# Kernel optimization log

Hardware: AMD Instinct MI355X
Metric: run time of the kernel (lower is better)

Reference implementation:

```python
import jax, jax.numpy as jnp
import numpy as np

S, N, E = 128, 512, 256   # msa depth, residues, msa embedding
P, C = 32, 128            # product embedding, pair embedding
EPS = 1e-5


def setup_inputs() -> dict:
    key = jax.random.key(0)
    ks = jax.random.split(key, 7)
    sc_e = 1.0 / np.sqrt(E)
    sc_p = 1.0 / np.sqrt(P)
    return {
        "msa_rep": jax.random.normal(ks[0], (S, N, E), dtype=jnp.float32),
        "ln_gamma": jnp.ones((E,), dtype=jnp.float32),
        "ln_beta": jnp.zeros((E,), dtype=jnp.float32),
        "Wa": jax.random.uniform(ks[1], (E, P), minval=-sc_e, maxval=sc_e, dtype=jnp.float32),
        "ba": jax.random.uniform(ks[2], (P,), minval=-sc_e, maxval=sc_e, dtype=jnp.float32),
        "Wb": jax.random.uniform(ks[3], (E, P), minval=-sc_e, maxval=sc_e, dtype=jnp.float32),
        "bb": jax.random.uniform(ks[4], (P,), minval=-sc_e, maxval=sc_e, dtype=jnp.float32),
        "Wp": jax.random.uniform(ks[5], (P, C), minval=-sc_p, maxval=sc_p, dtype=jnp.float32),
        "bp": jax.random.uniform(ks[6], (C,), minval=-sc_p, maxval=sc_p, dtype=jnp.float32),
    }


def reference(msa_rep, ln_gamma, ln_beta, Wa, ba, Wb, bb, Wp, bp):
    # LayerNorm over msa embedding dim
    mu = jnp.mean(msa_rep, axis=-1, keepdims=True)
    var = jnp.var(msa_rep, axis=-1, keepdims=True)
    x = (msa_rep - mu) / jnp.sqrt(var + EPS) * ln_gamma + ln_beta
    # dual projections: [S, N, P]
    a = x @ Wa + ba
    b = x @ Wb + bb
    # outer-product mean over MSA depth S without materializing [S, P, N, N]:
    # outer[n, m, p] = mean_s a[s, n, p] * b[s, m, p]  -> batched GEMM over p
    outer = jnp.einsum('snp,smp->nmp', a, b) / a.shape[0]
    # project product channels to pair embedding: [N, N, C]
    return outer @ Wp + bp
```

## Files before the change

kernel.cpp:

```cpp
#include <hip/hip_runtime.h>

#define S_DEPTH 128
#define N_RES   512
#define E_DIM   256
#define P_DIM   32
#define C_DIM   128

typedef short bh8 __attribute__((ext_vector_type(8)));
typedef float fx4 __attribute__((ext_vector_type(4)));

__device__ __forceinline__ unsigned short f2bf(float x){
    unsigned int u = __builtin_bit_cast(unsigned int, x);
    u += 0x7fffu + ((u >> 16) & 1u);
    return (unsigned short)(u >> 16);
}

__global__ void prep_kernel(const float* __restrict__ Wa, const float* __restrict__ Wb,
                            const float* __restrict__ Wp,
                            unsigned short* __restrict__ WaT, unsigned short* __restrict__ WbT,
                            unsigned short* __restrict__ WpT){
    int t = threadIdx.x;
    for (int i = 0; i < 32; ++i){
        int idx = i * 256 + t;
        int p = idx >> 8, e = idx & 255;
        WaT[idx] = f2bf(Wa[e * P_DIM + p]);
        WbT[idx] = f2bf(Wb[e * P_DIM + p]);
    }
    for (int i = 0; i < 16; ++i){
        int idx = i * 256 + t;
        int c = idx >> 5, p = idx & 31;
        WpT[idx] = f2bf(Wp[p * C_DIM + c]);
    }
}

__global__ __launch_bounds__(256) void lnproj_kernel(
    const float* __restrict__ x, const float* __restrict__ gamma, const float* __restrict__ beta,
    const unsigned short* __restrict__ WaT, const unsigned short* __restrict__ WbT,
    const float* __restrict__ ba, const float* __restrict__ bb,
    unsigned short* __restrict__ aT, unsigned short* __restrict__ bT)
{
    __shared__ __align__(16) char smem[S_DEPTH * E_DIM * 2];
    const int n0   = blockIdx.x;
    const int tid  = threadIdx.x;
    const int lane = tid & 63;
    const int w    = tid >> 6;
    const int l15  = lane & 15;
    const int lq   = lane >> 4;

    const float4 g4 = *(const float4*)(gamma + lane * 4);
    const float4 b4 = *(const float4*)(beta  + lane * 4);

    for (int rr = 0; rr < 32; ++rr){
        int s = w * 32 + rr;
        float4 v = *(const float4*)(x + ((size_t)(s * N_RES + n0)) * E_DIM + lane * 4);
        float sum = v.x + v.y + v.z + v.w;
        float sq  = v.x*v.x + v.y*v.y + v.z*v.z + v.w*v.w;
        #pragma unroll
        for (int m = 1; m < 64; m <<= 1){
            sum += __shfl_xor(sum, m);
            sq  += __shfl_xor(sq,  m);
        }
        float mu  = sum * (1.0f / E_DIM);
        float inv = rsqrtf(sq * (1.0f / E_DIM) - mu * mu + 1e-5f);
        ushort4 pk;
        pk.x = f2bf((v.x - mu) * inv * g4.x + b4.x);
        pk.y = f2bf((v.y - mu) * inv * g4.y + b4.y);
        pk.z = f2bf((v.z - mu) * inv * g4.z + b4.z);
        pk.w = f2bf((v.w - mu) * inv * g4.w + b4.w);
        int boff = s * 512 + lane * 8;
        boff ^= (s & 7) << 4;
        *(ushort4*)(smem + boff) = pk;
    }
    __syncthreads();

    fx4 accA[2][2], accB[2][2];
    #pragma unroll
    for (int st = 0; st < 2; ++st)
        #pragma unroll
        for (int pt = 0; pt < 2; ++pt){
            accA[st][pt] = fx4{0.f, 0.f, 0.f, 0.f};
            accB[st][pt] = fx4{0.f, 0.f, 0.f, 0.f};
        }

    #pragma unroll
    for (int ks = 0; ks < 8; ++ks){
        bh8 wa[2], wb[2];
        #pragma unroll
        for (int pt = 0; pt < 2; ++pt){
            int off = (pt * 16 + l15) * E_DIM + ks * 32 + lq * 8;
            wa[pt] = *(const bh8*)(WaT + off);
            wb[pt] = *(const bh8*)(WbT + off);
        }
        #pragma unroll
        for (int st = 0; st < 2; ++st){
            int srow = (w * 2 + st) * 16 + l15;
            int boff = srow * 512 + (ks * 32 + lq * 8) * 2;
            boff ^= (srow & 7) << 4;
            bh8 xf = *(const bh8*)(smem + boff);
            #pragma unroll
            for (int pt = 0; pt < 2; ++pt){
                accA[st][pt] = __builtin_amdgcn_mfma_f32_16x16x32_bf16(wa[pt], xf, accA[st][pt], 0, 0, 0);
                accB[st][pt] = __builtin_amdgcn_mfma_f32_16x16x32_bf16(wb[pt], xf, accB[st][pt], 0, 0, 0);
            }
        }
    }

    #pragma unroll
    for (int st = 0; st < 2; ++st){
        int s = (w * 2 + st) * 16 + l15;
        #pragma unroll
        for (int pt = 0; pt < 2; ++pt){
            #pragma unroll
            for (int j = 0; j < 4; ++j){
                int p = pt * 16 + lq * 4 + j;
                size_t o = ((size_t)p * N_RES + n0) * S_DEPTH + s;
                aT[o] = f2bf(accA[st][pt][j] + ba[p]);
                bT[o] = f2bf(accB[st][pt][j] + bb[p]);
            }
        }
    }
}

__global__ __launch_bounds__(512) void outer_kernel(
    const unsigned short* __restrict__ aT, const unsigned short* __restrict__ bT,
    const unsigned short* __restrict__ WpT, const float* __restrict__ bp,
    float* __restrict__ out)
{
    __shared__ __align__(16) char smem[1024 * 64];
    const int tn = blockIdx.x >> 4, tm = blockIdx.x & 15;
    const int n0 = tn * 32, m0 = tm * 32;
    const int tid  = threadIdx.x;
    const int lane = tid & 63;
    const int w    = tid >> 6;
    const int l15  = lane & 15;
    const int lq   = lane >> 4;

    #pragma unroll
    for (int q = 0; q < 4; ++q){
        int p = w * 4 + q;
        fx4 acc[2][2];
        #pragma unroll
        for (int ti = 0; ti < 2; ++ti)
            #pragma unroll
            for (int tj = 0; tj < 2; ++tj)
                acc[ti][tj] = fx4{0.f, 0.f, 0.f, 0.f};

        #pragma unroll
        for (int ks = 0; ks < 4; ++ks){
            bh8 af[2], bfv[2];
            #pragma unroll
            for (int t = 0; t < 2; ++t){
                af[t]  = *(const bh8*)(aT + ((size_t)p * N_RES + n0 + t * 16 + l15) * S_DEPTH + ks * 32 + lq * 8);
                bfv[t] = *(const bh8*)(bT + ((size_t)p * N_RES + m0 + t * 16 + l15) * S_DEPTH + ks * 32 + lq * 8);
            }
            #pragma unroll
            for (int ti = 0; ti < 2; ++ti)
                #pragma unroll
                for (int tj = 0; tj < 2; ++tj)
                    acc[ti][tj] = __builtin_amdgcn_mfma_f32_16x16x32_bf16(af[ti], bfv[tj], acc[ti][tj], 0, 0, 0);
        }
        #pragma unroll
        for (int ti = 0; ti < 2; ++ti)
            #pragma unroll
            for (int tj = 0; tj < 2; ++tj)
                #pragma unroll
                for (int j = 0; j < 4; ++j){
                    int nloc = ti * 16 + lq * 4 + j;
                    int mloc = tj * 16 + l15;
                    int nm = nloc * 32 + mloc;
                    *(unsigned short*)(smem + nm * 64 + p * 2) =
                        f2bf(acc[ti][tj][j] * (1.0f / S_DEPTH));
                }
    }
    __syncthreads();

    bh8   wpf[8];
    float bpv[8];
    #pragma unroll
    for (int ct = 0; ct < 8; ++ct){
        wpf[ct] = *(const bh8*)(WpT + (ct * 16 + l15) * P_DIM + lq * 8);
        bpv[ct] = bp[ct * 16 + l15];
    }
    #pragma unroll
    for (int mi = 0; mi < 8; ++mi){
        int mt = w * 8 + mi;
        bh8 of = *(const bh8*)(smem + (mt * 16 + l15) * 64 + lq * 16);
        #pragma unroll
        for (int ct = 0; ct < 8; ++ct){
            fx4 d = __builtin_amdgcn_mfma_f32_16x16x32_bf16(
                        of, wpf[ct], fx4{0.f, 0.f, 0.f, 0.f}, 0, 0, 0);
            #pragma unroll
            for (int j = 0; j < 4; ++j){
                int nm = mt * 16 + lq * 4 + j;
                int n = n0 + (nm >> 5), m = m0 + (nm & 31);
                out[((size_t)n * N_RES + m) * C_DIM + ct * 16 + l15] = d[j] + bpv[ct];
            }
        }
    }
}

extern "C" void kernel_launch(void* const* d_in, const int* in_sizes, int n_in,
                              void* d_out, int out_size, void* d_ws, size_t ws_size,
                              hipStream_t stream){
    const float* msa   = (const float*)d_in[0];
    const float* gamma = (const float*)d_in[1];
    const float* beta  = (const float*)d_in[2];
    const float* Wa    = (const float*)d_in[3];
    const float* ba    = (const float*)d_in[4];
    const float* Wb    = (const float*)d_in[5];
    const float* bb    = (const float*)d_in[6];
    const float* Wp    = (const float*)d_in[7];
    const float* bp    = (const float*)d_in[8];
    float* out = (float*)d_out;

    unsigned short* ws  = (unsigned short*)d_ws;
    unsigned short* aT  = ws;
    unsigned short* bT  = ws + 2097152;
    unsigned short* WaT = ws + 4194304;
    unsigned short* WbT = WaT + 8192;
    unsigned short* WpT = WbT + 8192;

    prep_kernel<<<1, 256, 0, stream>>>(Wa, Wb, Wp, WaT, WbT, WpT);
    lnproj_kernel<<<N_RES, 256, 0, stream>>>(msa, gamma, beta, WaT, WbT, ba, bb, aT, bT);
    outer_kernel<<<256, 512, 0, stream>>>(aT, bT, WpT, bp, out);
}
```

Before: 79.43 us.

## Retile all three kernels: parallel prep, split-S lnproj, 32x16 outer tiles

The prep kernel now runs on 48 blocks with one element per thread instead of a single serial block. The LN+projection kernel splits S across two blocks per residue and swaps the MFMA operand order so the output comes out as vectorized ushort4 stores. The outer kernel uses 32x16 tiles with 256 threads and grid swizzling, with each wave owning 8 product channels so the bf16 intermediate can be packed and written in 16-byte chunks into padded LDS. Output uses nontemporal stores with simpler addressing. These changes aim to raise occupancy, improve store coalescing and cut LDS write traffic, at the cost of more re-reading of the a/b operands per output tile.

Measured after the change: 102.5 us. 1.29x slower.

```diff
diff --git a/kernel.cpp b/kernel.cpp
--- a/kernel.cpp
+++ b/kernel.cpp
@@ -19,28 +19,27 @@
                             const float* __restrict__ Wp,
                             unsigned short* __restrict__ WaT, unsigned short* __restrict__ WbT,
                             unsigned short* __restrict__ WpT){
-    int t = threadIdx.x;
-    for (int i = 0; i < 32; ++i){
-        int idx = i * 256 + t;
-        int p = idx >> 8, e = idx & 255;
-        WaT[idx] = f2bf(Wa[e * P_DIM + p]);
-        WbT[idx] = f2bf(Wb[e * P_DIM + p]);
-    }
-    for (int i = 0; i < 16; ++i){
-        int idx = i * 256 + t;
-        int c = idx >> 5, p = idx & 31;
-        WpT[idx] = f2bf(Wp[p * C_DIM + c]);
-    }
-}
-
-__global__ __launch_bounds__(256) void lnproj_kernel(
+    int tid = blockIdx.x * 256 + threadIdx.x;
+    if (tid < 8192){
+        int p = tid >> 8, e = tid & 255;
+        WaT[tid] = f2bf(Wa[e * P_DIM + p]);
+        WbT[tid] = f2bf(Wb[e * P_DIM + p]);
+    } else {
+        int i = tid - 8192;
+        int c = i >> 5, p = i & 31;
+        WpT[i] = f2bf(Wp[p * C_DIM + c]);
+    }
+}
+
+__global__ __launch_bounds__(256, 4) void lnproj_kernel(
     const float* __restrict__ x, const float* __restrict__ gamma, const float* __restrict__ beta,
     const unsigned short* __restrict__ WaT, const unsigned short* __restrict__ WbT,
     const float* __restrict__ ba, const float* __restrict__ bb,
     unsigned short* __restrict__ aT, unsigned short* __restrict__ bT)
 {
-    __shared__ __align__(16) char smem[S_DEPTH * E_DIM * 2];
+    __shared__ __align__(16) char smem[64 * 512];
     const int n0   = blockIdx.x;
+    const int sh   = blockIdx.y;
     const int tid  = threadIdx.x;
     const int lane = tid & 63;
     const int w    = tid >> 6;
@@ -50,8 +49,9 @@
     const float4 g4 = *(const float4*)(gamma + lane * 4);
     const float4 b4 = *(const float4*)(beta  + lane * 4);
 
-    for (int rr = 0; rr < 32; ++rr){
-        int s = w * 32 + rr;
+    for (int rr = 0; rr < 16; ++rr){
+        int s_loc = w * 16 + rr;
+        int s     = sh * 64 + s_loc;
         float4 v = *(const float4*)(x + ((size_t)(s * N_RES + n0)) * E_DIM + lane * 4);
         float sum = v.x + v.y + v.z + v.w;
         float sq  = v.x*v.x + v.y*v.y + v.z*v.z + v.w*v.w;
@@ -67,111 +67,99 @@
         pk.y = f2bf((v.y - mu) * inv * g4.y + b4.y);
         pk.z = f2bf((v.z - mu) * inv * g4.z + b4.z);
         pk.w = f2bf((v.w - mu) * inv * g4.w + b4.w);
-        int boff = s * 512 + lane * 8;
-        boff ^= (s & 7) << 4;
+        int boff = s_loc * 512 + lane * 8;
+        boff ^= (s_loc & 7) << 4;
         *(ushort4*)(smem + boff) = pk;
     }
     __syncthreads();
 
-    fx4 accA[2][2], accB[2][2];
-    #pragma unroll
-    for (int st = 0; st < 2; ++st)
-        #pragma unroll
-        for (int pt = 0; pt < 2; ++pt){
-            accA[st][pt] = fx4{0.f, 0.f, 0.f, 0.f};
-            accB[st][pt] = fx4{0.f, 0.f, 0.f, 0.f};
-        }
+    fx4 accA[2], accB[2];
+    #pragma unroll
+    for (int pt = 0; pt < 2; ++pt){
+        accA[pt] = fx4{0.f, 0.f, 0.f, 0.f};
+        accB[pt] = fx4{0.f, 0.f, 0.f, 0.f};
+    }
+    const int srow = w * 16 + l15;
 
     #pragma unroll
     for (int ks = 0; ks < 8; ++ks){
-        bh8 wa[2], wb[2];
+        int boff = srow * 512 + (ks * 32 + lq * 8) * 2;
+        boff ^= (srow & 7) << 4;
+        bh8 xf = *(const bh8*)(smem + boff);
         #pragma unroll
         for (int pt = 0; pt < 2; ++pt){
             int off = (pt * 16 + l15) * E_DIM + ks * 32 + lq * 8;
-            wa[pt] = *(const bh8*)(WaT + off);
-            wb[pt] = *(const bh8*)(WbT + off);
-        }
-        #pragma unroll
-        for (int st = 0; st < 2; ++st){
-            int srow = (w * 2 + st) * 16 + l15;
-            int boff = srow * 512 + (ks * 32 + lq * 8) * 2;
-            boff ^= (srow & 7) << 4;
-            bh8 xf = *(const bh8*)(smem + boff);
-            #pragma unroll
-            for (int pt = 0; pt < 2; ++pt){
-                accA[st][pt] = __builtin_amdgcn_mfma_f32_16x16x32_bf16(wa[pt], xf, accA[st][pt], 0, 0, 0);
-                accB[st][pt] = __builtin_amdgcn_mfma_f32_16x16x32_bf16(wb[pt], xf, accB[st][pt], 0, 0, 0);
-            }
-        }
-    }
-
-    #pragma unroll
-    for (int st = 0; st < 2; ++st){
-        int s = (w * 2 + st) * 16 + l15;
-        #pragma unroll
-        for (int pt = 0; pt < 2; ++pt){
-            #pragma unroll
-            for (int j = 0; j < 4; ++j){
-                int p = pt * 16 + lq * 4 + j;
-                size_t o = ((size_t)p * N_RES + n0) * S_DEPTH + s;
-                aT[o] = f2bf(accA[st][pt][j] + ba[p]);
-                bT[o] = f2bf(accB[st][pt][j] + bb[p]);
-            }
-        }
-    }
-}
-
-__global__ __launch_bounds__(512) void outer_kernel(
+            bh8 wa = *(const bh8*)(WaT + off);
+            bh8 wb = *(const bh8*)(WbT + off);
+            accA[pt] = __builtin_amdgcn_mfma_f32_16x16x32_bf16(xf, wa, accA[pt], 0, 0, 0);
+            accB[pt] = __builtin_amdgcn_mfma_f32_16x16x32_bf16(xf, wb, accB[pt], 0, 0, 0);
+        }
+    }
+
+    #pragma unroll
+    for (int pt = 0; pt < 2; ++pt){
+        int p = pt * 16 + l15;
+        float bav = ba[p], bbv = bb[p];
+        int s_base = sh * 64 + w * 16 + lq * 4;
+        size_t o = ((size_t)p * N_RES + n0) * S_DEPTH + s_base;
+        ushort4 ua, ub;
+        ua.x = f2bf(accA[pt][0] + bav); ua.y = f2bf(accA[pt][1] + bav);
+        ua.z = f2bf(accA[pt][2] + bav); ua.w = f2bf(accA[pt][3] + bav);
+        ub.x = f2bf(accB[pt][0] + bbv); ub.y = f2bf(accB[pt][1] + bbv);
+        ub.z = f2bf(accB[pt][2] + bbv); ub.w = f2bf(accB[pt][3] + bbv);
+        *(ushort4*)(aT + o) = ua;
+        *(ushort4*)(bT + o) = ub;
+    }
+}
+
+__global__ __launch_bounds__(256, 2) void outer_kernel(
     const unsigned short* __restrict__ aT, const unsigned short* __restrict__ bT,
     const unsigned short* __restrict__ WpT, const float* __restrict__ bp,
     float* __restrict__ out)
 {
-    __shared__ __align__(16) char smem[1024 * 64];
-    const int tn = blockIdx.x >> 4, tm = blockIdx.x & 15;
-    const int n0 = tn * 32, m0 = tm * 32;
+    __shared__ __align__(16) char smem[512 * 80];
+    int bid = blockIdx.x;
+    int swz = (bid & 7) * 64 + (bid >> 3);
+    const int tn = swz >> 5, tm = swz & 31;
+    const int n0 = tn * 32, m0 = tm * 16;
     const int tid  = threadIdx.x;
     const int lane = tid & 63;
     const int w    = tid >> 6;
     const int l15  = lane & 15;
     const int lq   = lane >> 4;
 
-    #pragma unroll
-    for (int q = 0; q < 4; ++q){
-        int p = w * 4 + q;
-        fx4 acc[2][2];
+    fx4 acc[8][2];
+    #pragma unroll
+    for (int q = 0; q < 8; ++q)
         #pragma unroll
         for (int ti = 0; ti < 2; ++ti)
+            acc[q][ti] = fx4{0.f, 0.f, 0.f, 0.f};
+
+    #pragma unroll
+    for (int ks = 0; ks < 4; ++ks){
+        #pragma unroll
+        for (int q = 0; q < 8; ++q){
+            int p = w * 8 + q;
+            size_t kbase = (size_t)p * N_RES * S_DEPTH + ks * 32 + lq * 8;
+            bh8 bfv = *(const bh8*)(bT + kbase + (size_t)(m0 + l15) * S_DEPTH);
+            bh8 af0 = *(const bh8*)(aT + kbase + (size_t)(n0 + l15) * S_DEPTH);
+            bh8 af1 = *(const bh8*)(aT + kbase + (size_t)(n0 + 16 + l15) * S_DEPTH);
+            acc[q][0] = __builtin_amdgcn_mfma_f32_16x16x32_bf16(af0, bfv, acc[q][0], 0, 0, 0);
+            acc[q][1] = __builtin_amdgcn_mfma_f32_16x16x32_bf16(af1, bfv, acc[q][1], 0, 0, 0);
+        }
+    }
+
+    #pragma unroll
+    for (int ti = 0; ti < 2; ++ti)
+        #pragma unroll
+        for (int j = 0; j < 4; ++j){
+            int nm = (ti * 16 + lq * 4 + j) * 16 + l15;
+            bh8 v;
             #pragma unroll
-            for (int tj = 0; tj < 2; ++tj)
-                acc[ti][tj] = fx4{0.f, 0.f, 0.f, 0.f};
-
-        #pragma unroll
-        for (int ks = 0; ks < 4; ++ks){
-            bh8 af[2], bfv[2];
-            #pragma unroll
-            for (int t = 0; t < 2; ++t){
-                af[t]  = *(const bh8*)(aT + ((size_t)p * N_RES + n0 + t * 16 + l15) * S_DEPTH + ks * 32 + lq * 8);
-                bfv[t] = *(const bh8*)(bT + ((size_t)p * N_RES + m0 + t * 16 + l15) * S_DEPTH + ks * 32 + lq * 8);
-            }
-            #pragma unroll
-            for (int ti = 0; ti < 2; ++ti)
-                #pragma unroll
-                for (int tj = 0; tj < 2; ++tj)
-                    acc[ti][tj] = __builtin_amdgcn_mfma_f32_16x16x32_bf16(af[ti], bfv[tj], acc[ti][tj], 0, 0, 0);
-        }
-        #pragma unroll
-        for (int ti = 0; ti < 2; ++ti)
-            #pragma unroll
-            for (int tj = 0; tj < 2; ++tj)
-                #pragma unroll
-                for (int j = 0; j < 4; ++j){
-                    int nloc = ti * 16 + lq * 4 + j;
-                    int mloc = tj * 16 + l15;
-                    int nm = nloc * 32 + mloc;
-                    *(unsigned short*)(smem + nm * 64 + p * 2) =
-                        f2bf(acc[ti][tj][j] * (1.0f / S_DEPTH));
-                }
-    }
+            for (int q = 0; q < 8; ++q)
+                v[q] = (short)f2bf(acc[q][ti][j] * (1.0f / S_DEPTH));
+            *(bh8*)(smem + nm * 80 + w * 16) = v;
+        }
     __syncthreads();
 
     bh8   wpf[8];
@@ -184,17 +172,15 @@
     #pragma unroll
     for (int mi = 0; mi < 8; ++mi){
         int mt = w * 8 + mi;
-        bh8 of = *(const bh8*)(smem + (mt * 16 + l15) * 64 + lq * 16);
+        bh8 of = *(const bh8*)(smem + (mt * 16 + l15) * 80 + lq * 16);
         #pragma unroll
         for (int ct = 0; ct < 8; ++ct){
             fx4 d = __builtin_amdgcn_mfma_f32_16x16x32_bf16(
                         of, wpf[ct], fx4{0.f, 0.f, 0.f, 0.f}, 0, 0, 0);
+            float* po = out + (((size_t)(n0 + mt) * N_RES) + m0) * C_DIM + ct * 16 + l15;
             #pragma unroll
-            for (int j = 0; j < 4; ++j){
-                int nm = mt * 16 + lq * 4 + j;
-                int n = n0 + (nm >> 5), m = m0 + (nm & 31);
-                out[((size_t)n * N_RES + m) * C_DIM + ct * 16 + l15] = d[j] + bpv[ct];
-            }
+            for (int j = 0; j < 4; ++j)
+                __builtin_nontemporal_store(d[j] + bpv[ct], po + (size_t)(lq * 4 + j) * C_DIM);
         }
     }
 }
@@ -220,7 +206,7 @@
     unsigned short* WbT = WaT + 8192;
     unsigned short* WpT = WbT + 8192;
 
-    prep_kernel<<<1, 256, 0, stream>>>(Wa, Wb, Wp, WaT, WbT, WpT);
-    lnproj_kernel<<<N_RES, 256, 0, stream>>>(msa, gamma, beta, WaT, WbT, ba, bb, aT, bT);
-    outer_kernel<<<256, 512, 0, stream>>>(aT, bT, WpT, bp, out);
-}
+    prep_kernel<<<48, 256, 0, stream>>>(Wa, Wb, Wp, WaT, WbT, WpT);
+    lnproj_kernel<<<dim3(N_RES, 2), 256, 0, stream>>>(msa, gamma, beta, WaT, WbT, ba, bb, aT, bT);
+    outer_kernel<<<512, 256, 0, stream>>>(aT, bT, WpT, bp, out);
+}
```
